# Kernel tuning notes

Measured on AMD Instinct MI355X. Metric: run time of the kernel, lower is better.

Reference implementation:

```python
import jax, jax.numpy as jnp
import numpy as np
import math

DIM = 1024
CHUNK = 64
B, S = 4, 4096

def setup_inputs() -> dict:
    key = jax.random.key(0)
    ks = jax.random.split(key, 16)
    d = DIM
    std = 1.0 / math.sqrt(d)
    def lin(k):
        k1, k2 = jax.random.split(k)
        return (jax.random.uniform(k1, (d, d), jnp.float32, -std, std),
                jax.random.uniform(k2, (d,), jnp.float32, -std, std))
    Wk, bk = lin(ks[0])
    Wv, bv = lin(ks[1])
    Wq, bq = lin(ks[2])
    Wkp, bkp = lin(ks[3])
    Wqp, bqp = lin(ks[4])
    Wo, bo = lin(ks[5])
    return {
        "x": jax.random.normal(ks[6], (B, S, d), jnp.float32),
        "Wk": Wk, "bk": bk, "Wv": Wv, "bv": bv, "Wq": Wq, "bq": bq,
        "Wkp": Wkp, "bkp": bkp, "Wqp": Wqp, "bqp": bqp,
        "phase_scale": jnp.full((d,), math.pi, jnp.float32),
        "ln_g": jnp.ones((d,), jnp.float32),
        "ln_b": jnp.zeros((d,), jnp.float32),
        "Wo": Wo, "bo": bo,
    }

def _linear(x, W, b):
    # torch nn.Linear: x @ W.T + b
    return jnp.einsum('bsd,ed->bse', x, W) + b

def _layernorm(x, g, b, eps=1e-5):
    mu = jnp.mean(x, axis=-1, keepdims=True)
    var = jnp.var(x, axis=-1, keepdims=True)
    return (x - mu) * jax.lax.rsqrt(var + eps) * g + b

def reference(x, Wk, bk, Wv, bv, Wq, bq, Wkp, bkp, Wqp, bqp,
              phase_scale, ln_g, ln_b, Wo, bo):
    batch, seq_len, dim = x.shape
    key = _linear(x, Wk, bk)
    value = _linear(x, Wv, bv)
    query = _linear(x, Wq, bq)
    key_phase = jnp.tanh(_linear(key, Wkp, bkp)) * phase_scale
    query_phase = jnp.tanh(_linear(query, Wqp, bqp)) * phase_scale
    bound_real = value * jnp.cos(key_phase)
    bound_imag = value * jnpp_sin(key_phase) if False else value * jnp.sin(key_phase)
    pad_len = (CHUNK - seq_len % CHUNK) % CHUNK
    if pad_len > 0:
        pad = ((0, 0), (0, pad_len), (0, 0))
        bound_real = jnp.pad(bound_real, pad)
        bound_imag = jnp.pad(bound_imag, pad)
        query_phase = jnp.pad(query_phase, pad)
    padded_len = bound_real.shape[1]
    nc = padded_len // CHUNK
    br = bound_real.reshape(batch, nc, CHUNK, dim)
    bi = bound_imag.reshape(batch, nc, CHUNK, dim)
    qp = query_phase.reshape(batch, nc, CHUNK, dim)
    mem_real = jnp.cumsum(br, axis=2)
    mem_imag = jnp.cumsum(bi, axis=2)
    retrieved = mem_real * jnp.cos(qp) + mem_imag * jnp.sin(qp)
    retrieved = retrieved.reshape(batch, padded_len, dim)[:, :seq_len]
    retrieved = retrieved / math.sqrt(dim)
    out = _linear(_layernorm(retrieved, ln_g, ln_b), Wo, bo)
    return x + out
```

## Files before the change

kernel.cpp:

```cpp
#include <hip/hip_runtime.h>
#include <math.h>

#define DIMD 1024
#define CHUNKLEN 64
#define NTOK 16384

#define TM 128
#define TN 128
#define BK 64

typedef __bf16 bf16x8 __attribute__((ext_vector_type(8)));
typedef float floatx4 __attribute__((ext_vector_type(4)));
typedef unsigned short ushort8v __attribute__((ext_vector_type(8)));

__device__ __forceinline__ float bf2f(unsigned short u) {
  union { unsigned int i; float f; } v; v.i = ((unsigned int)u) << 16; return v.f;
}
__device__ __forceinline__ unsigned short f2bf(float f) {
  union { float f; unsigned int i; } v; v.f = f;
  unsigned int r = v.i + 0x7FFFu + ((v.i >> 16) & 1u);
  return (unsigned short)(r >> 16);
}

__device__ __forceinline__ float tanh_fast(float v) {
  const float t = __expf(2.0f * v);
  return 1.0f - 2.0f * __builtin_amdgcn_rcpf(t + 1.0f);
}

__device__ __forceinline__ void async16(const unsigned short* g, unsigned short* l) {
  __builtin_amdgcn_global_load_lds(
      (const __attribute__((address_space(1))) unsigned int*)g,
      (__attribute__((address_space(3))) unsigned int*)l, 16, 0, 0);
}

__global__ __launch_bounds__(256) void cvt_all_kernel(
    const float* __restrict__ x,
    const float* __restrict__ w0, const float* __restrict__ w1,
    const float* __restrict__ w2, const float* __restrict__ w3,
    unsigned short* __restrict__ dx,
    unsigned short* __restrict__ d0, unsigned short* __restrict__ d1,
    unsigned short* __restrict__ d2, unsigned short* __restrict__ d3)
{
  const int b = blockIdx.x;
  const float* src; unsigned short* dst; long i;
  if (b < 16384) {
    src = x; dst = dx; i = (long)b * 256 + threadIdx.x;
  } else {
    const int r = b - 16384;
    const int s = r >> 10;
    src = s == 0 ? w0 : s == 1 ? w1 : s == 2 ? w2 : w3;
    dst = s == 0 ? d0 : s == 1 ? d1 : s == 2 ? d2 : d3;
    i = (long)(r & 1023) * 256 + threadIdx.x;
  }
  const float4 v = ((const float4*)src)[i];
  ushort4 o;
  o.x = f2bf(v.x); o.y = f2bf(v.y); o.z = f2bf(v.z); o.w = f2bf(v.w);
  ((ushort4*)dst)[i] = o;
}

__global__ __launch_bounds__(256) void transpose_cvt_kernel(
    const float* __restrict__ s0, const float* __restrict__ s1,
    unsigned short* __restrict__ q0, unsigned short* __restrict__ q1)
{
  __shared__ unsigned short tile[64][66];
  const float* src = blockIdx.z ? s1 : s0;
  unsigned short* dst = blockIdx.z ? q1 : q0;
  const int e0 = blockIdx.y * 64;
  const int k0 = blockIdx.x * 64;
  const int t  = threadIdx.x;
  const int tr = t >> 4;
  const int tc = t & 15;
#pragma unroll
  for (int p = 0; p < 4; ++p) {
    const int el = p * 16 + tr;
    const float4 v = *(const float4*)&src[(long)(e0 + el) * DIMD + k0 + tc * 4];
    tile[el][tc * 4 + 0] = f2bf(v.x);
    tile[el][tc * 4 + 1] = f2bf(v.y);
    tile[el][tc * 4 + 2] = f2bf(v.z);
    tile[el][tc * 4 + 3] = f2bf(v.w);
  }
  __syncthreads();
#pragma unroll
  for (int p = 0; p < 4; ++p) {
    const int kl = p * 16 + tr;
    ushort4 o;
    o.x = tile[tc * 4 + 0][kl];
    o.y = tile[tc * 4 + 1][kl];
    o.z = tile[tc * 4 + 2][kl];
    o.w = tile[tc * 4 + 3][kl];
    *(ushort4*)&dst[(long)(k0 + kl) * DIMD + e0 + tc * 4] = o;
  }
}

__global__ __launch_bounds__(256) void bias_comb_kernel(
    const float* __restrict__ Wkp, const float* __restrict__ bk,
    const float* __restrict__ bkp,
    const float* __restrict__ Wqp, const float* __restrict__ bq,
    const float* __restrict__ bqp,
    float* __restrict__ bkq, float* __restrict__ bqq)
{
  const int b = blockIdx.x;
  const int which = b >> 8;
  const int lane = threadIdx.x & 63;
  const int wid  = threadIdx.x >> 6;
  const int n = (b & 255) * 4 + wid;
  const float* W    = which ? Wqp : Wkp;
  const float* bvec = which ? bq  : bk;
  const float* badd = which ? bqp : bkp;
  float*       outp = which ? bqq : bkq;
  float s = 0.f;
#pragma unroll
  for (int i = 0; i < 16; ++i)
    s += W[(long)n * DIMD + lane + i * 64] * bvec[lane + i * 64];
#pragma unroll
  for (int o = 32; o > 0; o >>= 1) s += __shfl_xor(s, o, 64);
  if (lane == 0) outp[n] = s + badd[n];
}

template <int MODE>
__global__ __launch_bounds__(256) void gemm_bt_kernel(
    const unsigned short* __restrict__ A0, const unsigned short* __restrict__ A1,
    const unsigned short* __restrict__ W0, const unsigned short* __restrict__ W1,
    const unsigned short* __restrict__ W2,
    const float* __restrict__ b0, const float* __restrict__ b1,
    const float* __restrict__ b2,
    const float* __restrict__ aux,
    unsigned short* __restrict__ O0, unsigned short* __restrict__ O1,
    unsigned short* __restrict__ O2,
    float* __restrict__ Of, const float* __restrict__ resid)
{
  __shared__ unsigned short lsA[TM * BK];
  __shared__ unsigned short lsB[TN * BK];

  const int tid  = threadIdx.x;
  const int lane = tid & 63;
  const int wid  = tid >> 6;
  const long bm  = (long)blockIdx.y * TM;
  const long bng = (long)blockIdx.x * TN;

  const unsigned short* A = A0;
  const unsigned short* W = W0;
  const float* bias = b0;
  unsigned short* Ob = O0;
  long bn = bng;
  int seg = 0;
  if (MODE == 0) {
    seg = (int)(bng >> 10);
    bn = bng & 1023;
    W    = seg == 0 ? W0 : (seg == 1 ? W1 : W2);
    bias = seg == 0 ? b0 : (seg == 1 ? b1 : b2);
    Ob   = seg == 0 ? O0 : (seg == 1 ? O1 : O2);
  } else if (MODE == 1) {
    if (blockIdx.z) { A = A1; W = W1; Ob = O1; }
  }

  const int wm = (wid & 1) * 64;
  const int wn = (wid >> 1) * 64;

  floatx4 acc[4][4];
#pragma unroll
  for (int i = 0; i < 4; ++i)
#pragma unroll
    for (int j = 0; j < 4; ++j)
      acc[i][j] = (floatx4)(0.0f);

  const int srow  = lane >> 3;
  const int pcol  = (lane & 7) * 8;
  const int lcolL = (((lane & 7) ^ (srow & 7)) * 8);
  const int frm   = lane & 15;
  const int cfrk  = lane >> 4;

  for (int kk = 0; kk < DIMD; kk += BK) {
    __syncthreads();
#pragma unroll
    for (int j = 0; j < 4; ++j) {
      const int inst = wid * 4 + j;
      const int r = inst * 8 + srow;
      async16(A + (bm + r) * (long)DIMD + kk + lcolL, &lsA[r * BK + pcol]);
      async16(W + (bn + r) * (long)DIMD + kk + lcolL, &lsB[r * BK + pcol]);
    }
    __syncthreads();
#pragma unroll
    for (int ks = 0; ks < BK; ks += 32) {
      const int cb  = (ks >> 3) + cfrk;
      const int swz = ((cb ^ (frm & 7)) << 3);
      bf16x8 af[4], bfr[4];
#pragma unroll
      for (int i = 0; i < 4; ++i)
        af[i]  = *(const bf16x8*)&lsA[(wm + i * 16 + frm) * BK + swz];
#pragma unroll
      for (int i = 0; i < 4; ++i)
        bfr[i] = *(const bf16x8*)&lsB[(wn + i * 16 + frm) * BK + swz];
#pragma unroll
      for (int i = 0; i < 4; ++i)
#pragma unroll
        for (int j = 0; j < 4; ++j)
          acc[i][j] = __builtin_amdgcn_mfma_f32_16x16x32_bf16(af[i], bfr[j], acc[i][j], 0, 0, 0);
    }
  }

  const int cn = lane & 15;
  const int rq = (lane >> 4) * 4;
#pragma unroll
  for (int j = 0; j < 4; ++j) {
    const long col = bn + wn + j * 16 + cn;
    const float bv = (MODE == 1) ? 0.0f : bias[col];
    const float pv = (MODE == 0) ? aux[col] : 0.0f;
#pragma unroll
    for (int i = 0; i < 4; ++i) {
#pragma unroll
      for (int r = 0; r < 4; ++r) {
        const long row = bm + wm + i * 16 + rq + r;
        const float v = acc[i][j][r] + bv;
        if (MODE == 0) {
          Ob[row * (long)DIMD + col] = (seg == 0) ? f2bf(v)
                                                  : f2bf(tanh_fast(v) * pv);
        } else if (MODE == 1) {
          Ob[row * (long)DIMD + col] = f2bf(v);
        } else {
          Of[row * (long)DIMD + col] = v + resid[row * (long)DIMD + col];
        }
      }
    }
  }
}

#define TILE16 16384
#define HALF16 8192

template <int MODE>
__global__ __launch_bounds__(512, 2) void gemm256_kernel(
    const unsigned short* __restrict__ A,
    const unsigned short* __restrict__ W0, const unsigned short* __restrict__ W1,
    const unsigned short* __restrict__ W2,
    const float* __restrict__ b0, const float* __restrict__ b1,
    const float* __restrict__ b2,
    const float* __restrict__ aux,
    unsigned short* __restrict__ O0, unsigned short* __restrict__ O1,
    unsigned short* __restrict__ O2,
    float* __restrict__ Of, const float* __restrict__ resid)
{
  __shared__ unsigned short lds[4 * TILE16];

  const int tid  = threadIdx.x;
  const int lane = tid & 63;
  const int wid  = tid >> 6;

  constexpr int NBX = (MODE == 0) ? 12 : 4;
  constexpr int NWG = NBX * 64;
  const int orig = blockIdx.x + blockIdx.y * gridDim.x;
  const int swzb = (orig & 7) * (NWG >> 3) + (orig >> 3);
  const int nb = swzb % NBX;
  const int mb = swzb / NBX;

  const long bm = (long)mb * 256;
  long bn;
  int seg = 0;
  const unsigned short* W = W0;
  const float* bias = b0;
  unsigned short* Ob = O0;
  if (MODE == 0) {
    seg = nb >> 2;
    bn  = (long)(nb & 3) * 256;
    W    = seg == 0 ? W0 : (seg == 1 ? W1 : W2);
    bias = seg == 0 ? b0 : (seg == 1 ? b1 : b2);
    Ob   = seg == 0 ? O0 : (seg == 1 ? O1 : O2);
  } else {
    bn = (long)nb * 256;
  }

  const int wm = (wid >> 2) * 128;
  const int wn = (wid & 3) * 64;

  const int q0  = wid * 2;
  const int sr0 = q0 * 16 + (lane >> 2);
  const int sg  = (((lane & 3) ^ ((sr0 >> 1) & 3)) * 8);
  const int sd0 = q0 * 512 + lane * 8;
  const long arow = (bm + sr0) * (long)DIMD;
  const long brow = (bn + sr0) * (long)DIMD;

  const int frm   = lane & 15;
  const int cfrk  = lane >> 4;
  const int slot8 = (cfrk ^ ((frm >> 1) & 3)) * 8;
  const int rbase = frm * 32 + slot8;

  floatx4 acc[8][4];
#pragma unroll
  for (int i = 0; i < 8; ++i)
#pragma unroll
    for (int j = 0; j < 4; ++j) acc[i][j] = (floatx4)(0.0f);

  bf16x8 bfr[4];

#define SA256(buf, kk, h) do { \
    const unsigned short* _s = A + arow + (kk) + (h) * 32 + sg; \
    unsigned short* _d = &lds[(buf) * TILE16 + (h) * HALF16 + sd0]; \
    async16(_s, _d); \
    async16(_s + 16 * DIMD, _d + 512); \
  } while (0)
#define SB256(buf, kk, h) do { \
    const unsigned short* _s = W + brow + (kk) + (h) * 32 + sg; \
    unsigned short* _d = &lds[2 * TILE16 + (buf) * TILE16 + (h) * HALF16 + sd0]; \
    async16(_s, _d); \
    async16(_s + 16 * DIMD, _d + 512); \
  } while (0)
#define RDA256(buf, h, ih, af) do { \
    const int _ab = (buf) * TILE16 + (h) * HALF16 + (wm + (ih) * 64) * 32 + rbase; \
    _Pragma("unroll") \
    for (int _i = 0; _i < 4; ++_i) (af)[_i] = *(const bf16x8*)&lds[_ab + _i * 512]; \
  } while (0)
#define RDB256(buf, h) do { \
    const int _bb = 2 * TILE16 + (buf) * TILE16 + (h) * HALF16 + wn * 32 + rbase; \
    _Pragma("unroll") \
    for (int _j = 0; _j < 4; ++_j) bfr[_j] = *(const bf16x8*)&lds[_bb + _j * 512]; \
  } while (0)
#define VMW4() asm volatile("s_waitcnt vmcnt(4)" ::: "memory")
#define BAR256() do { \
    asm volatile("" ::: "memory"); \
    __builtin_amdgcn_s_barrier(); \
    asm volatile("" ::: "memory"); \
  } while (0)
#define MFMA16(ih, af) do { \
    __builtin_amdgcn_s_setprio(1); \
    _Pragma("unroll") \
    for (int _i = 0; _i < 4; ++_i) \
      _Pragma("unroll") \
      for (int _j = 0; _j < 4; ++_j) \
        acc[(ih) * 4 + _i][_j] = __builtin_amdgcn_mfma_f32_16x16x32_bf16( \
            (af)[_i], bfr[_j], acc[(ih) * 4 + _i][_j], 0, 0, 0); \
    __builtin_amdgcn_s_setprio(0); \
  } while (0)
#define KTILE(c, n, kn) do { \
    { bf16x8 af[4]; RDA256(c, 0, 0, af); RDB256(c, 0); \
      SA256(n, kn, 0); MFMA16(0, af); } \
    { bf16x8 af[4]; RDA256(c, 0, 1, af); \
      SB256(n, kn, 0); VMW4(); BAR256(); MFMA16(1, af); } \
    { bf16x8 af[4]; RDA256(c, 1, 0, af); RDB256(c, 1); \
      SA256(n, kn, 1); MFMA16(0, af); } \
    { bf16x8 af[4]; RDA256(c, 1, 1, af); \
      SB256(n, kn, 1); VMW4(); BAR256(); MFMA16(1, af); } \
  } while (0)

  SA256(0, 0, 0); SB256(0, 0, 0); SA256(0, 0, 1); SB256(0, 0, 1);
  VMW4();
  BAR256();

#pragma unroll 1
  for (int t = 0; t < 16; t += 2) {
    const int k1 = (t + 1) * 64;
    const int k2 = (t + 2 < 16) ? (t + 2) * 64 : 0;
    KTILE(0, 1, k1);
    KTILE(1, 0, k2);
  }
  asm volatile("s_waitcnt vmcnt(0)" ::: "memory");

#undef SA256
#undef SB256
#undef RDA256
#undef RDB256
#undef VMW4
#undef BAR256
#undef MFMA16
#undef KTILE

  const int cn = lane & 15;
  const int rq = (lane >> 4) * 4;
  long colj[4]; float bvj[4], pvj[4];
#pragma unroll
  for (int j = 0; j < 4; ++j) {
    colj[j] = bn + wn + j * 16 + cn;
    bvj[j]  = bias[colj[j]];
    pvj[j]  = (MODE == 0) ? aux[colj[j]] : 0.0f;
  }
#pragma unroll
  for (int ii = 0; ii < 8; ++ii) {
#pragma unroll
    for (int r = 0; r < 4; ++r) {
      const long rowo = (bm + wm + ii * 16 + rq + r) * (long)DIMD;
#pragma unroll
      for (int j = 0; j < 4; ++j) {
        const float v = acc[ii][j][r] + bvj[j];
        if (MODE == 0) {
          Ob[rowo + colj[j]] = (seg == 0) ? f2bf(v)
                                          : f2bf(tanh_fast(v) * pvj[j]);
        } else {
          Of[rowo + colj[j]] = v + resid[rowo + colj[j]];
        }
      }
    }
  }
}

__global__ __launch_bounds__(512) void scan_ln_kernel(
    const unsigned short* __restrict__ V,  const unsigned short* __restrict__ KP,
    const unsigned short* __restrict__ QP,
    const float* __restrict__ lng, const float* __restrict__ lnb,
    unsigned short* __restrict__ out)
{
  __shared__ unsigned short ret_s[32][DIMD];

  const int tid  = threadIdx.x;
  const int lane = tid & 63;
  const int wid  = tid >> 6;
  const long rowBase = (long)blockIdx.x * CHUNKLEN;
  const int d0 = tid * 2;

  const int c0 = lane * 8;
  const int c1 = 512 + lane * 8;
  float g0[8], be0[8], g1[8], be1[8];
#pragma unroll
  for (int j = 0; j < 8; ++j) {
    g0[j] = lng[c0 + j]; be0[j] = lnb[c0 + j];
    g1[j] = lng[c1 + j]; be1[j] = lnb[c1 + j];
  }

  float mr[2] = {0.f, 0.f};
  float mi[2] = {0.f, 0.f};

  for (int h = 0; h < 2; ++h) {
    for (int tl = 0; tl < 32; ++tl) {
      const int t = h * 32 + tl;
      const long off = (rowBase + t) * DIMD + d0;
      const ushort2 v2 = *(const ushort2*)(V + off);
      const ushort2 k2 = *(const ushort2*)(KP + off);
      const ushort2 q2 = *(const ushort2*)(QP + off);
      const unsigned short va[2] = {v2.x, v2.y};
      const unsigned short ka[2] = {k2.x, k2.y};
      const unsigned short qa[2] = {q2.x, q2.y};
      unsigned short rv[2];
#pragma unroll
      for (int j = 0; j < 2; ++j) {
        const float v  = bf2f(va[j]);
        const float kp = bf2f(ka[j]);
        const float qp = bf2f(qa[j]);
        float skp, ckp, sqp, cqp;
        __sincosf(kp, &skp, &ckp);
        __sincosf(qp, &sqp, &cqp);
        mr[j] += v * ckp;
        mi[j] += v * skp;
        rv[j] = f2bf((mr[j] * cqp + mi[j] * sqp) * 0.03125f);
      }
      ushort2 o2; o2.x = rv[0]; o2.y = rv[1];
      *(ushort2*)&ret_s[tl][d0] = o2;
    }
    __syncthreads();

#pragma unroll 1
    for (int rr = 0; rr < 4; ++rr) {
      const int tl = wid * 4 + rr;
      const ushort8v a0 = *(const ushort8v*)&ret_s[tl][c0];
      const ushort8v a1 = *(const ushort8v*)&ret_s[tl][c1];
      float f0[8], f1[8];
      float s = 0.f, s2 = 0.f;
#pragma unroll
      for (int j = 0; j < 8; ++j) {
        f0[j] = bf2f(a0[j]); f1[j] = bf2f(a1[j]);
        s += f0[j] + f1[j];
        s2 += f0[j] * f0[j] + f1[j] * f1[j];
      }
#pragma unroll
      for (int o = 32; o > 0; o >>= 1) {
        s  += __shfl_xor(s,  o, 64);
        s2 += __shfl_xor(s2, o, 64);
      }
      const float mu  = s * (1.0f / DIMD);
      const float var = s2 * (1.0f / DIMD) - mu * mu;
      const float inv = rsqrtf(var + 1e-5f);
      ushort8v o0, o1;
#pragma unroll
      for (int j = 0; j < 8; ++j) {
        o0[j] = f2bf((f0[j] - mu) * inv * g0[j] + be0[j]);
        o1[j] = f2bf((f1[j] - mu) * inv * g1[j] + be1[j]);
      }
      const long gro = (rowBase + h * 32 + tl) * DIMD;
      *(ushort8v*)(out + gro + c0) = o0;
      *(ushort8v*)(out + gro + c1) = o1;
    }
    __syncthreads();
  }
}

extern "C" void kernel_launch(void* const* d_in, const int* in_sizes, int n_in,
                              void* d_out, int out_size, void* d_ws, size_t ws_size,
                              hipStream_t stream)
{
  const float* x   = (const float*)d_in[0];
  const float* Wk  = (const float*)d_in[1];
  const float* bk  = (const float*)d_in[2];
  const float* Wv  = (const float*)d_in[3];
  const float* bv  = (const float*)d_in[4];
  const float* Wq  = (const float*)d_in[5];
  const float* bq  = (const float*)d_in[6];
  const float* Wkp = (const float*)d_in[7];
  const float* bkp = (const float*)d_in[8];
  const float* Wqp = (const float*)d_in[9];
  const float* bqp = (const float*)d_in[10];
  const float* ph  = (const float*)d_in[11];
  const float* lng = (const float*)d_in[12];
  const float* lnb = (const float*)d_in[13];
  const float* Wo  = (const float*)d_in[14];
  const float* bo  = (const float*)d_in[15];
  float* out = (float*)d_out;

  const long NB = (long)NTOK * DIMD;
  const long DD = (long)DIMD * DIMD;
  const size_t required = (size_t)(4 * NB + 8 * DD) * sizeof(unsigned short)
                        + 2048 * sizeof(float);
  if (ws_size < required) return;

  unsigned short* S0   = (unsigned short*)d_ws;
  unsigned short* SV   = S0   + NB;
  unsigned short* SKP  = SV   + NB;
  unsigned short* SQP  = SKP  + NB;
  unsigned short* Wvb  = SQP  + NB;
  unsigned short* Wob  = Wvb  + DD;
  unsigned short* Wkpb = Wob  + DD;
  unsigned short* Wqpb = Wkpb + DD;
  unsigned short* WkT  = Wqpb + DD;
  unsigned short* WqT  = WkT  + DD;
  unsigned short* Wkqb = WqT  + DD;
  unsigned short* Wqqb = Wkqb + DD;
  float* bkq = (float*)(Wqqb + DD);
  float* bqq = bkq + DIMD;

  dim3 blk(256);

  cvt_all_kernel<<<dim3(16384 + 4 * 1024), blk, 0, stream>>>(
      x, Wv, Wo, Wkp, Wqp, S0, Wvb, Wob, Wkpb, Wqpb);
  transpose_cvt_kernel<<<dim3(16, 16, 2), blk, 0, stream>>>(Wk, Wq, WkT, WqT);
  bias_comb_kernel<<<dim3(512), blk, 0, stream>>>(Wkp, bk, bkp, Wqp, bq, bqp, bkq, bqq);
  gemm_bt_kernel<1><<<dim3(DIMD / TN, DIMD / TM, 2), blk, 0, stream>>>(
      Wkpb, Wqpb, WkT, WqT, nullptr, nullptr, nullptr, nullptr, nullptr,
      Wkqb, Wqqb, nullptr, nullptr, nullptr);
  gemm256_kernel<0><<<dim3(12, NTOK / 256), dim3(512), 0, stream>>>(
      S0, Wvb, Wkqb, Wqqb, bv, bkq, bqq, ph, SV, SKP, SQP, nullptr, nullptr);
  scan_ln_kernel<<<dim3(NTOK / CHUNKLEN), dim3(512), 0, stream>>>(
      SV, SKP, SQP, lng, lnb, S0);
  gemm256_kernel<2><<<dim3(4, NTOK / 256), dim3(512), 0, stream>>>(
      S0, Wob, nullptr, nullptr, bo, nullptr, nullptr, nullptr,
      nullptr, nullptr, nullptr, out, x);
}
```

Measured before the change: 358.9 us.

## Software-pipeline scan loads and use hardware sin/cos with pre-scaled phase

Folds the 1/(2π) factor into the phase scale in the GEMM epilogue so the scan kernel can call the raw hardware sin/cos instructions, which take input in revolutions, instead of __sincosf. The chunk scan now double-buffers global loads of V, KP and QP eight tokens at a time, so the next batch's loads are in flight while the current batch is computed. This targets memory latency and transcendental instruction cost in the retrieval/layernorm kernel, at the price of more registers. The stored phase values are now in revolutions, so any other consumer of them must expect that convention.

```diff
diff --git a/kernel.cpp b/kernel.cpp
--- a/kernel.cpp
+++ b/kernel.cpp
@@ -8,6 +8,8 @@
 #define TM 128
 #define TN 128
 #define BK 64
+
+#define INV2PI 0.15915494309189535f
 
 typedef __bf16 bf16x8 __attribute__((ext_vector_type(8)));
 typedef float floatx4 __attribute__((ext_vector_type(4)));
@@ -370,7 +372,7 @@
   for (int j = 0; j < 4; ++j) {
     colj[j] = bn + wn + j * 16 + cn;
     bvj[j]  = bias[colj[j]];
-    pvj[j]  = (MODE == 0) ? aux[colj[j]] : 0.0f;
+    pvj[j]  = (MODE == 0) ? aux[colj[j]] * INV2PI : 0.0f;
   }
 #pragma unroll
   for (int ii = 0; ii < 8; ++ii) {
@@ -417,67 +419,95 @@
   float mr[2] = {0.f, 0.f};
   float mi[2] = {0.f, 0.f};
 
-  for (int h = 0; h < 2; ++h) {
-    for (int tl = 0; tl < 32; ++tl) {
-      const int t = h * 32 + tl;
-      const long off = (rowBase + t) * DIMD + d0;
-      const ushort2 v2 = *(const ushort2*)(V + off);
-      const ushort2 k2 = *(const ushort2*)(KP + off);
-      const ushort2 q2 = *(const ushort2*)(QP + off);
-      const unsigned short va[2] = {v2.x, v2.y};
-      const unsigned short ka[2] = {k2.x, k2.y};
-      const unsigned short qa[2] = {q2.x, q2.y};
-      unsigned short rv[2];
-#pragma unroll
-      for (int j = 0; j < 2; ++j) {
-        const float v  = bf2f(va[j]);
-        const float kp = bf2f(ka[j]);
-        const float qp = bf2f(qa[j]);
-        float skp, ckp, sqp, cqp;
-        __sincosf(kp, &skp, &ckp);
-        __sincosf(qp, &sqp, &cqp);
-        mr[j] += v * ckp;
-        mi[j] += v * skp;
-        rv[j] = f2bf((mr[j] * cqp + mi[j] * sqp) * 0.03125f);
-      }
-      ushort2 o2; o2.x = rv[0]; o2.y = rv[1];
-      *(ushort2*)&ret_s[tl][d0] = o2;
-    }
-    __syncthreads();
-
-#pragma unroll 1
-    for (int rr = 0; rr < 4; ++rr) {
-      const int tl = wid * 4 + rr;
-      const ushort8v a0 = *(const ushort8v*)&ret_s[tl][c0];
-      const ushort8v a1 = *(const ushort8v*)&ret_s[tl][c1];
-      float f0[8], f1[8];
-      float s = 0.f, s2 = 0.f;
-#pragma unroll
-      for (int j = 0; j < 8; ++j) {
-        f0[j] = bf2f(a0[j]); f1[j] = bf2f(a1[j]);
-        s += f0[j] + f1[j];
-        s2 += f0[j] * f0[j] + f1[j] * f1[j];
-      }
-#pragma unroll
-      for (int o = 32; o > 0; o >>= 1) {
-        s  += __shfl_xor(s,  o, 64);
-        s2 += __shfl_xor(s2, o, 64);
-      }
-      const float mu  = s * (1.0f / DIMD);
-      const float var = s2 * (1.0f / DIMD) - mu * mu;
-      const float inv = rsqrtf(var + 1e-5f);
-      ushort8v o0, o1;
-#pragma unroll
-      for (int j = 0; j < 8; ++j) {
-        o0[j] = f2bf((f0[j] - mu) * inv * g0[j] + be0[j]);
-        o1[j] = f2bf((f1[j] - mu) * inv * g1[j] + be1[j]);
-      }
-      const long gro = (rowBase + h * 32 + tl) * DIMD;
-      *(ushort8v*)(out + gro + c0) = o0;
-      *(ushort8v*)(out + gro + c1) = o1;
-    }
-    __syncthreads();
-  }
+  ushort2 aV[8], aK[8], aQ[8];
+  ushort2 bV[8], bK[8], bQ[8];
+
+#define LOADG(BV, BK_, BQ, t8) do { \
+    _Pragma("unroll") \
+    for (int _u = 0; _u < 8; ++_u) { \
+      const long _o = (rowBase + (t8) + _u) * DIMD + d0; \
+      BV[_u]  = *(const ushort2*)(V  + _o); \
+      BK_[_u] = *(const ushort2*)(KP + _o); \
+      BQ[_u]  = *(const ushort2*)(QP + _o); \
+    } \
+  } while (0)
+#define COMP8(BV, BK_, BQ, lr0) do { \
+    _Pragma("unroll") \
+    for (int _u = 0; _u < 8; ++_u) { \
+      const unsigned short _va[2] = {BV[_u].x, BV[_u].y}; \
+      const unsigned short _ka[2] = {BK_[_u].x, BK_[_u].y}; \
+      const unsigned short _qa[2] = {BQ[_u].x, BQ[_u].y}; \
+      unsigned short _rv[2]; \
+      _Pragma("unroll") \
+      for (int _j = 0; _j < 2; ++_j) { \
+        const float _v  = bf2f(_va[_j]); \
+        const float _kp = bf2f(_ka[_j]); \
+        const float _qp = bf2f(_qa[_j]); \
+        const float _skp = __builtin_amdgcn_sinf(_kp); \
+        const float _ckp = __builtin_amdgcn_cosf(_kp); \
+        const float _sqp = __builtin_amdgcn_sinf(_qp); \
+        const float _cqp = __builtin_amdgcn_cosf(_qp); \
+        mr[_j] += _v * _ckp; \
+        mi[_j] += _v * _skp; \
+        _rv[_j] = f2bf((mr[_j] * _cqp + mi[_j] * _sqp) * 0.03125f); \
+      } \
+      ushort2 _o2; _o2.x = _rv[0]; _o2.y = _rv[1]; \
+      *(ushort2*)&ret_s[(lr0) + _u][d0] = _o2; \
+    } \
+  } while (0)
+#define LNPH2(hb) do { \
+    _Pragma("unroll 1") \
+    for (int rr = 0; rr < 4; ++rr) { \
+      const int tl = wid * 4 + rr; \
+      const ushort8v a0 = *(const ushort8v*)&ret_s[tl][c0]; \
+      const ushort8v a1 = *(const ushort8v*)&ret_s[tl][c1]; \
+      float f0[8], f1[8]; \
+      float s = 0.f, s2 = 0.f; \
+      _Pragma("unroll") \
+      for (int j = 0; j < 8; ++j) { \
+        f0[j] = bf2f(a0[j]); f1[j] = bf2f(a1[j]); \
+        s += f0[j] + f1[j]; \
+        s2 += f0[j] * f0[j] + f1[j] * f1[j]; \
+      } \
+      _Pragma("unroll") \
+      for (int o = 32; o > 0; o >>= 1) { \
+        s  += __shfl_xor(s,  o, 64); \
+        s2 += __shfl_xor(s2, o, 64); \
+      } \
+      const float mu  = s * (1.0f / DIMD); \
+      const float var = s2 * (1.0f / DIMD) - mu * mu; \
+      const float inv = rsqrtf(var + 1e-5f); \
+      ushort8v o0, o1; \
+      _Pragma("unroll") \
+      for (int j = 0; j < 8; ++j) { \
+        o0[j] = f2bf((f0[j] - mu) * inv * g0[j] + be0[j]); \
+        o1[j] = f2bf((f1[j] - mu) * inv * g1[j] + be1[j]); \
+      } \
+      const long gro = (rowBase + (hb) + tl) * DIMD; \
+      *(ushort8v*)(out + gro + c0) = o0; \
+      *(ushort8v*)(out + gro + c1) = o1; \
+    } \
+  } while (0)
+
+  LOADG(aV, aK, aQ, 0);
+  LOADG(bV, bK, bQ, 8);  COMP8(aV, aK, aQ, 0);
+  LOADG(aV, aK, aQ, 16); COMP8(bV, bK, bQ, 8);
+  LOADG(bV, bK, bQ, 24); COMP8(aV, aK, aQ, 16);
+  LOADG(aV, aK, aQ, 32); COMP8(bV, bK, bQ, 24);
+  __syncthreads();
+  LNPH2(0);
+  __syncthreads();
+  LOADG(bV, bK, bQ, 40); COMP8(aV, aK, aQ, 0);
+  LOADG(aV, aK, aQ, 48); COMP8(bV, bK, bQ, 8);
+  LOADG(bV, bK, bQ, 56); COMP8(aV, aK, aQ, 16);
+                         COMP8(bV, bK, bQ, 24);
+  __syncthreads();
+  LNPH2(32);
+  __syncthreads();
+
+#undef LOADG
+#undef COMP8
+#undef LNPH2
 }
 
 extern "C" void kernel_launch(void* const* d_in, const int* in_sizes, int n_in,
```

After: 365.1 us. Within noise of the previous version (+1.7%).
